# Performance work log

Hardware: AMD Instinct MI355X
Metric: run time of the kernel (lower is better)

Reference implementation:

```python
import jax, jax.numpy as jnp
import numpy as np

N, K, M, H, F = 4, 1024, 1024, 16, 4096
D = M // H  # per-head dim (dim_q = dim_v = 64)
EPS = 1e-5


def _mha(q_in, k_in, v_in, Wq, bq, Wk, bk, Wv, bv, Wo, bo, mask):
    # Wq/Wk/Wv: [H, M, D]; bq/bk/bv: [H, D]; Wo: [H*D, M]; bo: [M]
    q = jnp.einsum('nkm,hmd->nhkd', q_in, Wq) + bq[None, :, None, :]
    k = jnp.einsum('nkm,hmd->nhkd', k_in, Wk) + bk[None, :, None, :]
    v = jnp.einsum('nkm,hmd->nhkd', v_in, Wv) + bv[None, :, None, :]
    scores = jnp.einsum('nhkd,nhld->nhkl', q, k) / jnp.sqrt(jnp.asarray(D, q.dtype))
    if mask is not None:
        scores = jnp.where(mask[:, None, :, :] == 0, jnp.asarray(-jnp.inf, q.dtype), scores)
    attn = jax.nn.softmax(scores, axis=-1)          # [N,H,K,K]
    y = jnp.einsum('nhkl,nhld->nhkd', attn, v)      # [N,H,K,D]
    y = y.transpose(0, 2, 1, 3).reshape(q_in.shape[0], q_in.shape[1], -1)  # concat heads -> [N,K,H*D]
    return y @ Wo + bo


def _ln(x, g, b):
    mu = jnp.mean(x, axis=-1, keepdims=True)
    var = jnp.mean((x - mu) ** 2, axis=-1, keepdims=True)
    return (x - mu) * jax.lax.rsqrt(var + EPS) * g + b


def setup_inputs() -> dict:
    key = jax.random.key(0)
    ks = jax.random.split(key, 24)
    s = 0.02
    def rn(k, shape):
        return jax.random.normal(k, shape, dtype=jnp.float32) * s
    inp = {
        'dec_inp': jax.random.normal(ks[0], (N, K, M), dtype=jnp.float32),
        'enc_out': jax.random.normal(ks[1], (N, K, M), dtype=jnp.float32),
        'mask': jnp.tril(jnp.ones((K, K), dtype=jnp.int32))[None].repeat(N, axis=0),
        # self-attention params
        'Wq_s': rn(ks[2], (H, M, D)), 'bq_s': jnp.zeros((H, D)),
        'Wk_s': rn(ks[3], (H, M, D)), 'bk_s': jnp.zeros((H, D)),
        'Wv_s': rn(ks[4], (H, M, D)), 'bv_s': jnp.zeros((H, D)),
        'Wo_s': rn(ks[5], (H * D, M)), 'bo_s': jnp.zeros((M,)),
        # cross-attention params
        'Wq_c': rn(ks[6], (H, M, D)), 'bq_c': jnp.zeros((H, D)),
        'Wk_c': rn(ks[7], (H, M, D)), 'bk_c': jnp.zeros((H, D)),
        'Wv_c': rn(ks[8], (H, M, D)), 'bv_c': jnp.zeros((H, D)),
        'Wo_c': rn(ks[9], (H * D, M)), 'bo_c': jnp.zeros((M,)),
        # feedforward params
        'W1': rn(ks[10], (M, F)), 'b1': jnp.zeros((F,)),
        'W2': rn(ks[11], (F, M)), 'b2': jnp.zeros((M,)),
        # layernorm params
        'g1': jnp.ones((M,)), 'be1': jnp.zeros((M,)),
        'g2': jnp.ones((M,)), 'be2': jnp.zeros((M,)),
        'g3': jnp.ones((M,)), 'be3': jnp.zeros((M,)),
    }
    return inp


def reference(dec_inp, enc_out, mask,
              Wq_s, bq_s, Wk_s, bk_s, Wv_s, bv_s, Wo_s, bo_s,
              Wq_c, bq_c, Wk_c, bk_c, Wv_c, bv_c, Wo_c, bo_c,
              W1, b1, W2, b2, g1, be1, g2, be2, g3, be3):
    # masked self-attention + residual + LN (dropout = identity in eval)
    out1 = _mha(dec_inp, dec_inp, dec_inp, Wq_s, bq_s, Wk_s, bk_s, Wv_s, bv_s, Wo_s, bo_s, mask)
    out2 = _ln(dec_inp + out1, g1, be1)
    # cross-attention with encoder output + residual + LN
    out3 = _mha(out2, enc_out, enc_out, Wq_c, bq_c, Wk_c, bk_c, Wv_c, bv_c, Wo_c, bo_c, None)
    out4 = _ln(out3 + out2, g2, be2)
    # feedforward + residual + LN
    out5 = jax.nn.relu(out4 @ W1 + b1) @ W2 + b2
    return _ln(out5 + out4, g3, be3)
```

## Files before the change

### kernel.cpp

```cpp
#include <hip/hip_runtime.h>

#define NB   4
#define SEQ  1024
#define MD   1024
#define NH   16
#define HD   64
#define FF   4096
#define NK   (NB*SEQ)
#define EPSF 1e-5f
#define QS   3072

typedef short short8 __attribute__((ext_vector_type(8)));
typedef float f32x4  __attribute__((ext_vector_type(4)));
typedef unsigned short u16;
typedef unsigned int u32;

__device__ __forceinline__ u16 f2bf(float x) {
    union { float f; unsigned u; } v; v.f = x;
    unsigned r = v.u + 0x7FFF + ((v.u >> 16) & 1);
    return (u16)(r >> 16);
}
__device__ __forceinline__ u16 f2bf_trunc(float x) {
    union { float f; unsigned u; } v; v.f = x;
    return (u16)(v.u >> 16);
}
__device__ __forceinline__ float bf2f(u16 x) {
    union { unsigned u; float f; } v; v.u = ((unsigned)x) << 16;
    return v.f;
}
__device__ __forceinline__ void gload_lds16(const void* g, void* l) {
    __builtin_amdgcn_global_load_lds(
        (const __attribute__((address_space(1))) unsigned int*)g,
        (__attribute__((address_space(3))) unsigned int*)l,
        16, 0, 0);
}

__global__ __launch_bounds__(256) void conv_bf16(const float* __restrict__ s0,
                                                 const float* __restrict__ s1,
                                                 u16* __restrict__ d0,
                                                 u16* __restrict__ d1) {
    const float* S = blockIdx.y ? s1 : s0;
    u16* D = blockIdx.y ? d1 : d0;
    const int i = blockIdx.x * 256 + threadIdx.x;
    float4 v = ((const float4*)S)[i];
    ushort4 o;
    o.x = f2bf(v.x); o.y = f2bf(v.y); o.z = f2bf(v.z); o.w = f2bf(v.w);
    ((ushort4*)D)[i] = o;
}

__global__ __launch_bounds__(256) void mask_tiles(const int* __restrict__ mask,
                                                  int* __restrict__ cls,
                                                  u32* __restrict__ bits) {
    const int jt = blockIdx.x, qt = blockIdx.y, n = blockIdx.z;
    const int t = threadIdx.x;
    const int r = t >> 1, h2 = (t & 1) * 2;
    u32 bb[2];
#pragma unroll
    for (int sg = 0; sg < 2; ++sg) {
        const int* mp = &mask[((size_t)n * SEQ + qt * 128 + r) * SEQ + jt * 128 + (h2 + sg) * 32];
        u32 b = 0;
#pragma unroll
        for (int k = 0; k < 8; ++k) {
            int4 v = *(const int4*)(mp + k * 4);
            b |= (v.x ? 1u : 0u) << (k * 4 + 0);
            b |= (v.y ? 1u : 0u) << (k * 4 + 1);
            b |= (v.z ? 1u : 0u) << (k * 4 + 2);
            b |= (v.w ? 1u : 0u) << (k * 4 + 3);
        }
        bb[sg] = b;
    }
    const int tile = (n * 8 + qt) * 8 + jt;
    bits[((size_t)tile * 128 + r) * 4 + h2]     = bb[0];
    bits[((size_t)tile * 128 + r) * 4 + h2 + 1] = bb[1];
    const int nfull  = __syncthreads_count(bb[0] == 0xFFFFFFFFu && bb[1] == 0xFFFFFFFFu);
    const int nempty = __syncthreads_count(bb[0] == 0u && bb[1] == 0u);
    if (t == 0) cls[tile] = (nfull == 256) ? 2 : ((nempty == 256) ? 0 : 1);
}

struct QkvArgs { const float* src[6]; u16* dst[6]; };

__global__ __launch_bounds__(256) void repack_qkv(QkvArgs a) {
    const int m0 = blockIdx.x * 64;
    const int h  = blockIdx.y;
    const int w  = blockIdx.z;
    const float* W = a.src[w];
    u16* BT = a.dst[w];
    const int t = threadIdx.x;
    __shared__ u16 Ts[64][72];

    const int r = t >> 4, c4 = (t & 15) * 4;
#pragma unroll
    for (int p = 0; p < 4; ++p) {
        const int row = r + p * 16;
        float4 v = *(const float4*)&W[((size_t)h * 1024 + m0 + row) * 64 + c4];
        Ts[row][c4] = f2bf(v.x); Ts[row][c4 + 1] = f2bf(v.y);
        Ts[row][c4 + 2] = f2bf(v.z); Ts[row][c4 + 3] = f2bf(v.w);
    }
    __syncthreads();
    const int d = t >> 2, j0 = (t & 3) * 16;
#pragma unroll
    for (int p = 0; p < 4; ++p) {
        ushort4 o;
        o.x = Ts[j0 + p * 4 + 0][d]; o.y = Ts[j0 + p * 4 + 1][d];
        o.z = Ts[j0 + p * 4 + 2][d]; o.w = Ts[j0 + p * 4 + 3][d];
        *(ushort4*)&BT[((size_t)h * 64 + d) * 1024 + m0 + j0 + p * 4] = o;
    }
}

struct FD { const float* src; int ss; u16* dst; int ds; };
struct FlatArgs { FD d[10]; };

__global__ __launch_bounds__(256) void repack_flat(FlatArgs fa) {
    FD u = fa.d[blockIdx.z];
    const int r0 = blockIdx.x * 64;
    const int c0 = blockIdx.y * 64;
    const int t  = threadIdx.x;
    __shared__ u16 Ts[64][72];

    const int r = t >> 4, c4 = (t & 15) * 4;
#pragma unroll
    for (int p = 0; p < 4; ++p) {
        const int row = r + p * 16;
        float4 v = *(const float4*)&u.src[(size_t)(r0 + row) * u.ss + c0 + c4];
        Ts[row][c4] = f2bf(v.x); Ts[row][c4 + 1] = f2bf(v.y);
        Ts[row][c4 + 2] = f2bf(v.z); Ts[row][c4 + 3] = f2bf(v.w);
    }
    __syncthreads();
    const int d = t >> 2, j0 = (t & 3) * 16;
#pragma unroll
    for (int p = 0; p < 4; ++p) {
        ushort4 o;
        o.x = Ts[j0 + p * 4 + 0][d]; o.y = Ts[j0 + p * 4 + 1][d];
        o.z = Ts[j0 + p * 4 + 2][d]; o.w = Ts[j0 + p * 4 + 3][d];
        *(ushort4*)&u.dst[(size_t)(c0 + d) * u.ds + r0 + j0 + p * 4] = o;
    }
}

template<int OUT_BF16, int RELU, int RESID, int BIAS3, int PARTIAL, int VT>
__global__ __launch_bounds__(256) void gemm_mfma(const u16* __restrict__ A,
                                                 const u16* __restrict__ A2,
                                                 int Astride,
                                                 const u16* __restrict__ BT,
                                                 int Bstride,
                                                 const float* __restrict__ b0,
                                                 const float* __restrict__ b1p,
                                                 const float* __restrict__ b2p,
                                                 const float* __restrict__ resid,
                                                 void* __restrict__ Cout,
                                                 u16* __restrict__ VtOut,
                                                 int Kd, int Nd) {
    const int nt = blockIdx.x;
    const int mt = blockIdx.y;
    const int t  = threadIdx.x;
    const int wave = t >> 6, lane = t & 63;
    const int q = lane >> 4, l16 = lane & 15;
    const int wm = wave >> 1, wn = wave & 1;

    __shared__ __align__(16) u16 As[128 * 64];
    __shared__ __align__(16) u16 Bs[128 * 64];

    const int row0 = mt * 128, col0 = nt * 128;
    const u16* Ause = (col0 < 1024) ? A : A2;
    const int kBase = PARTIAL ? blockIdx.z * Kd : 0;

    f32x4 acc[4][4];
#pragma unroll
    for (int r = 0; r < 4; ++r)
#pragma unroll
        for (int c = 0; c < 4; ++c) acc[r][c] = (f32x4)0.0f;

    const int lrow = lane >> 3;
    const int lcb  = lane & 7;

    for (int k0 = 0; k0 < Kd; k0 += 64) {
        __syncthreads();
#pragma unroll
        for (int p = 0; p < 4; ++p) {
            const int rr = wave * 32 + p * 8 + lrow;
            const int gcb = lcb ^ (rr & 7);
            gload_lds16(Ause + (size_t)(row0 + rr) * Astride + kBase + k0 + gcb * 8, As + (size_t)(wave * 32 + p * 8) * 64);
            gload_lds16(BT   + (size_t)(col0 + rr) * Bstride + kBase + k0 + gcb * 8, Bs + (size_t)(wave * 32 + p * 8) * 64);
        }
        __syncthreads();

#pragma unroll
        for (int s = 0; s < 2; ++s) {
            const int pb = (q + s * 4) ^ (l16 & 7);
            short8 af[4], bf[4];
#pragma unroll
            for (int r = 0; r < 4; ++r)
                af[r] = *(const short8*)&As[(wm * 64 + r * 16 + l16) * 64 + pb * 8];
#pragma unroll
            for (int c = 0; c < 4; ++c)
                bf[c] = *(const short8*)&Bs[(wn * 64 + c * 16 + l16) * 64 + pb * 8];
#pragma unroll
            for (int r = 0; r < 4; ++r)
#pragma unroll
                for (int c = 0; c < 4; ++c)
                    acc[r][c] = __builtin_amdgcn_mfma_f32_16x16x32_bf16(af[r], bf[c], acc[r][c], 0, 0, 0);
        }
    }

    float* Pout = PARTIAL ? ((float*)Cout + (size_t)blockIdx.z * NK * Nd) : nullptr;

#pragma unroll
    for (int c = 0; c < 4; ++c) {
        const int col = col0 + wn * 64 + c * 16 + l16;
        float bb = 0.0f;
        if (!PARTIAL) {
            if (BIAS3) {
                const int sec = col >> 10;
                const float* bp = sec == 0 ? b0 : (sec == 1 ? b1p : b2p);
                bb = bp[col & 1023];
            } else {
                bb = b0[col];
            }
        }
#pragma unroll
        for (int r = 0; r < 4; ++r) {
#pragma unroll
            for (int reg = 0; reg < 4; ++reg) {
                const int row = row0 + wm * 64 + r * 16 + q * 4 + reg;
                float v = acc[r][c][reg] + bb;
                if (PARTIAL) {
                    Pout[(size_t)row * Nd + col] = acc[r][c][reg];
                } else {
                    if (RELU)  v = fmaxf(v, 0.0f);
                    if (RESID) v += resid[(size_t)row * Nd + col];
                    if (OUT_BF16) ((u16*)Cout)[(size_t)row * Nd + col] = f2bf(v);
                    else          ((float*)Cout)[(size_t)row * Nd + col] = v;
                }
            }
        }
    }
}

template<int OUT_BF16, int RELU, int BIAS3, int PARTIAL, int VT>
__global__ __launch_bounds__(512, 2) void gemm256(const u16* __restrict__ A,
                                                  const u16* __restrict__ A2,
                                                  int Astride,
                                                  const u16* __restrict__ BT,
                                                  int Bstride,
                                                  const float* __restrict__ b0,
                                                  const float* __restrict__ b1p,
                                                  const float* __restrict__ b2p,
                                                  void* __restrict__ Cout,
                                                  u16* __restrict__ VtOut,
                                                  int Kd, int Nd) {
    const int nt = blockIdx.x;
    const int mt = blockIdx.y;
    const int t  = threadIdx.x;
    const int wave = t >> 6, lane = t & 63;
    const int q = lane >> 4, l16 = lane & 15;
    const int wm = wave >> 2, wn = wave & 3;

    extern __shared__ __align__(16) char smem[];
    u16* As = (u16*)smem;
    u16* Bs = (u16*)(smem + 2 * 256 * 64 * 2);

    const int row0 = mt * 256, col0 = nt * 256;
    const u16* Ause = (col0 < 1024) ? A : A2;
    const int kBase = PARTIAL ? blockIdx.z * Kd : 0;

    f32x4 acc[8][4];
#pragma unroll
    for (int r = 0; r < 8; ++r)
#pragma unroll
        for (int c = 0; c < 4; ++c) acc[r][c] = (f32x4)0.0f;

    const int lrow = lane >> 3;
    const int lcb  = lane & 7;

    auto stage = [&](int buf, int kk) {
#pragma unroll
        for (int p = 0; p < 4; ++p) {
            const int rr = wave * 32 + p * 8 + lrow;
            const int gcb = lcb ^ (rr & 7);
            gload_lds16(Ause + (size_t)(row0 + rr) * Astride + kk + gcb * 8,
                        As + (size_t)buf * (256 * 64) + (wave * 32 + p * 8) * 64);
            gload_lds16(BT   + (size_t)(col0 + rr) * Bstride + kk + gcb * 8,
                        Bs + (size_t)buf * (256 * 64) + (wave * 32 + p * 8) * 64);
        }
    };

    const int nsteps = Kd / 64;
    stage(0, kBase);
    __syncthreads();

    int cur = 0;
    for (int it = 0; it < nsteps; ++it) {
        if (it + 1 < nsteps) stage(cur ^ 1, kBase + (it + 1) * 64);

        const u16* Ab = As + (size_t)cur * (256 * 64);
        const u16* Bb = Bs + (size_t)cur * (256 * 64);
#pragma unroll
        for (int s = 0; s < 2; ++s) {
            const int pb = (q + s * 4) ^ (l16 & 7);
            short8 af[8], bf[4];
#pragma unroll
            for (int r = 0; r < 8; ++r)
                af[r] = *(const short8*)&Ab[(wm * 128 + r * 16 + l16) * 64 + pb * 8];
#pragma unroll
            for (int c = 0; c < 4; ++c)
                bf[c] = *(const short8*)&Bb[(wn * 64 + c * 16 + l16) * 64 + pb * 8];
#pragma unroll
            for (int r = 0; r < 8; ++r)
#pragma unroll
                for (int c = 0; c < 4; ++c)
                    acc[r][c] = __builtin_amdgcn_mfma_f32_16x16x32_bf16(af[r], bf[c], acc[r][c], 0, 0, 0);
        }
        __syncthreads();
        cur ^= 1;
    }

    if (VT && col0 >= 2048) {
#pragma unroll
        for (int c = 0; c < 4; ++c) {
            const int col = col0 + wn * 64 + c * 16 + l16;
            const float bb = b2p[col & 1023];
            const int d = col & 63, hh = (col >> 6) & 15;
#pragma unroll
            for (int r = 0; r < 8; ++r) {
                const int row = row0 + wm * 128 + r * 16 + q * 4;
                const int nn = row >> 10, k = row & 1023;
                ushort4 o;
                o.x = f2bf(acc[r][c][0] + bb);
                o.y = f2bf(acc[r][c][1] + bb);
                o.z = f2bf(acc[r][c][2] + bb);
                o.w = f2bf(acc[r][c][3] + bb);
                *(ushort4*)&VtOut[((size_t)(nn * 16 + hh) * 64 + d) * 1024 + k] = o;
            }
        }
        return;
    }

    float* Pout = PARTIAL ? ((float*)Cout + (size_t)blockIdx.z * NK * Nd) : nullptr;

#pragma unroll
    for (int c = 0; c < 4; ++c) {
        const int col = col0 + wn * 64 + c * 16 + l16;
        float bb = 0.0f;
        if (!PARTIAL) {
            if (BIAS3) {
                const int sec = col >> 10;
                const float* bp = sec == 0 ? b0 : (sec == 1 ? b1p : b2p);
                bb = bp[col & 1023];
            } else {
                bb = b0[col];
            }
        }
#pragma unroll
        for (int r = 0; r < 8; ++r) {
#pragma unroll
            for (int reg = 0; reg < 4; ++reg) {
                const int row = row0 + wm * 128 + r * 16 + q * 4 + reg;
                float v = acc[r][c][reg] + bb;
                if (PARTIAL) {
                    Pout[(size_t)row * Nd + col] = acc[r][c][reg];
                } else {
                    if (RELU)  v = fmaxf(v, 0.0f);
                    if (OUT_BF16) ((u16*)Cout)[(size_t)row * Nd + col] = f2bf(v);
                    else          ((float*)Cout)[(size_t)row * Nd + col] = v;
                }
            }
        }
    }
}

#define PSTR 136
#define ATTN_LDS (128*64*2 + 64*128*2 + 8*16*PSTR*2)

__global__ __launch_bounds__(512, 4) void attn_mfma(const u16* __restrict__ QKV,
                                                    const u16* __restrict__ Vt,
                                                    const int* __restrict__ cls,
                                                    const u32* __restrict__ bits,
                                                    u16* __restrict__ Yout) {
    const int qt = blockIdx.x;
    const int h  = blockIdx.y;
    const int n  = blockIdx.z;
    const int t  = threadIdx.x;
    const int wave = t >> 6;
    const int lane = t & 63;
    const int quad = lane >> 4;
    const int l16  = lane & 15;
    const int sw   = wave >> 2;
    const int wq   = wave & 3;

    extern __shared__ __align__(16) char smem[];
    u16* Ks = (u16*)smem;
    u16* Vs = (u16*)(smem + 128 * 64 * 2);
    u16* Pw = (u16*)(smem + 128 * 64 * 2 + 64 * 128 * 2) + wave * 16 * PSTR;

    const int bh = n * NH + h;
    const int i0 = qt * 128;

    int cl[8];
    if (cls) {
        const int* cp = &cls[(n * 8 + qt) * 8];
#pragma unroll
        for (int j = 0; j < 8; ++j) cl[j] = cp[j];
    } else {
#pragma unroll
        for (int j = 0; j < 8; ++j) cl[j] = 2;
    }

    short8 qf[2];
    {
        const u16* qrow = QKV + ((size_t)n * SEQ + i0 + sw * 64 + wq * 16 + l16) * QS + h * 64 + quad * 8;
        short8 a = *(const short8*)(qrow);
        short8 b = *(const short8*)(qrow + 32);
#pragma unroll
        for (int j = 0; j < 8; ++j) {
            qf[0][j] = (short)f2bf(bf2f((u16)a[j]) * 0.18033688f);
            qf[1][j] = (short)f2bf(bf2f((u16)b[j]) * 0.18033688f);
        }
    }

    f32x4 O[4];
#pragma unroll
    for (int d = 0; d < 4; ++d) O[d] = (f32x4)0.0f;
    float lrow[4] = {};

    const int krow = lane >> 3, kblk = lane & 7;
    const int vrow = lane >> 4, vblk = lane & 15;
    const int x7 = l16 & 7;

    for (int jt = 0; jt < SEQ / 128; ++jt) {
        const int c = cl[jt];
        if (c == 0) continue;
        __syncthreads();

#pragma unroll
        for (int p = 0; p < 2; ++p) {
            const int rr = wave * 16 + p * 8 + krow;
            const int kb = kblk ^ (rr & 7);
            gload_lds16(QKV + ((size_t)n * SEQ + jt * 128 + rr) * QS + 1024 + h * 64 + kb * 8,
                        Ks + (wave * 16 + p * 8) * 64);
        }
#pragma unroll
        for (int p = 0; p < 2; ++p) {
            const int rr = wave * 8 + p * 4 + vrow;
            const int kb = vblk ^ (rr & 15);
            gload_lds16(Vt + ((size_t)bh * HD + rr) * SEQ + jt * 128 + kb * 8,
                        Vs + (wave * 8 + p * 4) * 128);
        }
        __syncthreads();

        f32x4 S[8];
#pragma unroll
        for (int sub = 0; sub < 8; ++sub) {
            S[sub] = (f32x4)0.0f;
            const int row = sub * 16 + l16;
            short8 k0 = *(const short8*)&Ks[row * 64 + ((quad ^ x7) * 8)];
            S[sub] = __builtin_amdgcn_mfma_f32_16x16x32_bf16(qf[0], k0, S[sub], 0, 0, 0);
            short8 k1 = *(const short8*)&Ks[row * 64 + (((4 + quad) ^ x7) * 8)];
            S[sub] = __builtin_amdgcn_mfma_f32_16x16x32_bf16(qf[1], k1, S[sub], 0, 0, 0);
        }

        if (c == 1) {
#pragma unroll
            for (int reg = 0; reg < 4; ++reg) {
                const int row = sw * 64 + wq * 16 + quad * 4 + reg;
                const uint4 mm = *(const uint4*)&bits[((size_t)((n * 8 + qt) * 8 + jt) * 128 + row) * 4];
#pragma unroll
                for (int sub = 0; sub < 8; ++sub) {
                    const u32 seg = (sub >> 1) == 0 ? mm.x : (sub >> 1) == 1 ? mm.y : (sub >> 1) == 2 ? mm.z : mm.w;
                    if (!((seg >> ((sub & 1) * 16 + l16)) & 1u)) S[sub][reg] = -1e30f;
                }
            }
        }

#pragma unroll
        for (int reg = 0; reg < 4; ++reg) {
            float rs = 0.0f;
#pragma unroll
            for (int sub = 0; sub < 8; ++sub) {
                float e = exp2f(S[sub][reg]);
                Pw[(quad * 4 + reg) * PSTR + sub * 16 + l16] = f2bf_trunc(e);
                rs += e;
            }
            rs += __shfl_xor(rs, 1);
            rs += __shfl_xor(rs, 2);
            rs += __shfl_xor(rs, 4);
            rs += __shfl_xor(rs, 8);
            lrow[reg] += rs;
        }

        short8 pa[4];
#pragma unroll
        for (int ks = 0; ks < 4; ++ks)
            pa[ks] = *(const short8*)&Pw[l16 * PSTR + ks * 32 + quad * 8];
#pragma unroll
        for (int d = 0; d < 4; ++d) {
            const int row = d * 16 + l16;
#pragma unroll
            for (int ks = 0; ks < 4; ++ks) {
                short8 vb = *(const short8*)&Vs[row * 128 + (((ks * 4 + quad) ^ l16) & 15) * 8];
                O[d] = __builtin_amdgcn_mfma_f32_16x16x32_bf16(pa[ks], vb, O[d], 0, 0, 0);
            }
        }
    }

#pragma unroll
    for (int d = 0; d < 4; ++d) {
#pragma unroll
        for (int reg = 0; reg < 4; ++reg) {
            const int row = i0 + sw * 64 + wq * 16 + quad * 4 + reg;
            const int col = h * 64 + d * 16 + l16;
            Yout[((size_t)n * SEQ + row) * QS + col] = f2bf(O[d][reg] / lrow[reg]);
        }
    }
}

__global__ __launch_bounds__(256) void ln_kernel(const float* __restrict__ X,
                                                 const float* __restrict__ g,
                                                 const float* __restrict__ be,
                                                 float* __restrict__ Y,
                                                 u16* __restrict__ Yb) {
    const int row = blockIdx.x;
    const int t = threadIdx.x;
    __shared__ float red[256];

    const float4 v = ((const float4*)(X + (size_t)row * MD))[t];
    red[t] = v.x + v.y + v.z + v.w;
    __syncthreads();
    for (int s2 = 128; s2 > 0; s2 >>= 1) {
        if (t < s2) red[t] += red[t + s2];
        __syncthreads();
    }
    const float mu = red[0] * (1.0f / MD);
    __syncthreads();

    float dx = v.x - mu, dy = v.y - mu, dz = v.z - mu, dw = v.w - mu;
    red[t] = dx * dx + dy * dy + dz * dz + dw * dw;
    __syncthreads();
    for (int s2 = 128; s2 > 0; s2 >>= 1) {
        if (t < s2) red[t] += red[t + s2];
        __syncthreads();
    }
    const float var = red[0] * (1.0f / MD);
    const float rs = rsqrtf(var + EPSF);

    const float4 gv = ((const float4*)g)[t];
    const float4 bv = ((const float4*)be)[t];
    float4 o;
    o.x = dx * rs * gv.x + bv.x;
    o.y = dy * rs * gv.y + bv.y;
    o.z = dz * rs * gv.z + bv.z;
    o.w = dw * rs * gv.w + bv.w;
    if (Y) ((float4*)(Y + (size_t)row * MD))[t] = o;
    if (Yb) {
        ushort4 ob;
        ob.x = f2bf(o.x); ob.y = f2bf(o.y); ob.z = f2bf(o.z); ob.w = f2bf(o.w);
        ((ushort4*)(Yb + (size_t)row * MD))[t] = ob;
    }
}

__global__ __launch_bounds__(256) void ln_fused2(const float* __restrict__ p0,
                                                 const float* __restrict__ p1,
                                                 const float* __restrict__ bias,
                                                 const float* __restrict__ resid,
                                                 const float* __restrict__ g,
                                                 const float* __restrict__ be,
                                                 float* __restrict__ Y) {
    const int row = blockIdx.x;
    const int t = threadIdx.x;
    __shared__ float red[256];

    const float4 a = ((const float4*)(p0 + (size_t)row * MD))[t];
    const float4 b = ((const float4*)(p1 + (size_t)row * MD))[t];
    const float4 r = ((const float4*)(resid + (size_t)row * MD))[t];
    const float4 bi = ((const float4*)bias)[t];
    float4 v;
    v.x = a.x + b.x + r.x + bi.x;
    v.y = a.y + b.y + r.y + bi.y;
    v.z = a.z + b.z + r.z + bi.z;
    v.w = a.w + b.w + r.w + bi.w;

    red[t] = v.x + v.y + v.z + v.w;
    __syncthreads();
    for (int s2 = 128; s2 > 0; s2 >>= 1) {
        if (t < s2) red[t] += red[t + s2];
        __syncthreads();
    }
    const float mu = red[0] * (1.0f / MD);
    __syncthreads();

    float dx = v.x - mu, dy = v.y - mu, dz = v.z - mu, dw = v.w - mu;
    red[t] = dx * dx + dy * dy + dz * dz + dw * dw;
    __syncthreads();
    for (int s2 = 128; s2 > 0; s2 >>= 1) {
        if (t < s2) red[t] += red[t + s2];
        __syncthreads();
    }
    const float var = red[0] * (1.0f / MD);
    const float rs = rsqrtf(var + EPSF);

    const float4 gv = ((const float4*)g)[t];
    const float4 bv = ((const float4*)be)[t];
    float4 o;
    o.x = dx * rs * gv.x + bv.x;
    o.y = dy * rs * gv.y + bv.y;
    o.z = dz * rs * gv.z + bv.z;
    o.w = dw * rs * gv.w + bv.w;
    ((float4*)(Y + (size_t)row * MD))[t] = o;
}

extern "C" void kernel_launch(void* const* d_in, const int* in_sizes, int n_in,
                              void* d_out, int out_size, void* d_ws, size_t ws_size,
                              hipStream_t stream) {
    const float* dec  = (const float*)d_in[0];
    const float* enc  = (const float*)d_in[1];
    const int*   mask = (const int*)d_in[2];
    const float* Wq_s = (const float*)d_in[3];
    const float* bq_s = (const float*)d_in[4];
    const float* Wk_s = (const float*)d_in[5];
    const float* bk_s = (const float*)d_in[6];
    const float* Wv_s = (const float*)d_in[7];
    const float* bv_s = (const float*)d_in[8];
    const float* Wo_s = (const float*)d_in[9];
    const float* bo_s = (const float*)d_in[10];
    const float* Wq_c = (const float*)d_in[11];
    const float* bq_c = (const float*)d_in[12];
    const float* Wk_c = (const float*)d_in[13];
    const float* bk_c = (const float*)d_in[14];
    const float* Wv_c = (const float*)d_in[15];
    const float* bv_c = (const float*)d_in[16];
    const float* Wo_c = (const float*)d_in[17];
    const float* bo_c = (const float*)d_in[18];
    const float* W1   = (const float*)d_in[19];
    const float* b1   = (const float*)d_in[20];
    const float* W2   = (const float*)d_in[21];
    const float* b2   = (const float*)d_in[22];
    const float* g1   = (const float*)d_in[23];
    const float* be1  = (const float*)d_in[24];
    const float* g2   = (const float*)d_in[25];
    const float* be2  = (const float*)d_in[26];
    const float* g3   = (const float*)d_in[27];
    const float* be3  = (const float*)d_in[28];

    char* wsb = (char*)d_ws;
    const size_t MB = 1u << 20;
    u16*   decb  = (u16*)(wsb + 0 * MB);
    u16*   O2b   = (u16*)(wsb + 0 * MB);
    u16*   encb  = (u16*)(wsb + 8 * MB);
    u16*   O4b   = (u16*)(wsb + 8 * MB);
    u16*   WqkvsT= (u16*)(wsb + 16 * MB);
    u16*   WqkvcT= (u16*)(wsb + 22 * MB);
    u16*   WosT  = (u16*)(wsb + 28 * MB);
    u16*   WocT  = (u16*)(wsb + 30 * MB);
    u16*   W1T   = (u16*)(wsb + 32 * MB);
    u16*   W2T   = (u16*)(wsb + 40 * MB);
    u16*   QKVb  = (u16*)(wsb + 48 * MB);
    u16*   Vt    = (u16*)(wsb + 72 * MB);
    u16*   Hb    = (u16*)(wsb + 48 * MB);
    int*   mcls  = (int*)(wsb + 80 * MB);
    u32*   mbits = (u32*)(wsb + 80 * MB + 64 * 1024);
    float* Tb    = (float*)(wsb + 80 * MB);
    float* FP    = (float*)(wsb + 0 * MB);
    float* O2    = (float*)(wsb + 96 * MB);
    float* O4    = (float*)(wsb + 96 * MB);

    dim3 blk(256);
    dim3 blkA(512);
    dim3 blkG(512);
    dim3 gConv(NK * MD / 4 / 256, 2);
    dim3 gMask(8, 8, 4);
    dim3 gQkvW(16, 16, 6);
    dim3 gFlatW(16, 16, 10);
    dim3 gAttn(SEQ / 128, NH, NB);
    dim3 gQKV(QS / 256, NK / 256);
    dim3 gOut(MD / 128, NK / 128);
    dim3 gF1(FF / 256, NK / 256);
    dim3 gF2(MD / 256, NK / 256, 2);
    const int G256_LDS = 2 * 2 * 256 * 64 * 2;

    conv_bf16<<<gConv, blk, 0, stream>>>(dec, enc, decb, encb);
    mask_tiles<<<gMask, blk, 0, stream>>>(mask, mcls, mbits);

    QkvArgs qa;
    qa.src[0] = Wq_s; qa.src[1] = Wk_s; qa.src[2] = Wv_s;
    qa.src[3] = Wq_c; qa.src[4] = Wk_c; qa.src[5] = Wv_c;
    qa.dst[0] = WqkvsT;                 qa.dst[1] = WqkvsT + (size_t)1024 * 1024;
    qa.dst[2] = WqkvsT + (size_t)2048 * 1024;
    qa.dst[3] = WqkvcT;                 qa.dst[4] = WqkvcT + (size_t)1024 * 1024;
    qa.dst[5] = WqkvcT + (size_t)2048 * 1024;
    repack_qkv<<<gQkvW, blk, 0, stream>>>(qa);

    FlatArgs fa;
    fa.d[0] = { Wo_s, 1024, WosT, 1024 };
    fa.d[1] = { Wo_c, 1024, WocT, 1024 };
    for (int u = 0; u < 4; ++u)
        fa.d[2 + u] = { W1 + (size_t)u * 1024, 4096, W1T + (size_t)u * 1024 * 1024, 1024 };
    for (int u = 0; u < 4; ++u)
        fa.d[6 + u] = { W2 + (size_t)u * 1024 * 1024, 1024, W2T + (size_t)u * 1024, 4096 };
    repack_flat<<<gFlatW, blk, 0, stream>>>(fa);

    gemm256<1, 0, 1, 0, 1><<<gQKV, blkG, G256_LDS, stream>>>(decb, decb, MD, WqkvsT, MD, bq_s, bk_s, bv_s, QKVb, Vt, MD, QS);
    attn_mfma<<<gAttn, blkA, ATTN_LDS, stream>>>(QKVb, Vt, mcls, mbits, QKVb);
    gemm_mfma<0, 0, 1, 0, 0, 0><<<gOut, blk, 0, stream>>>(QKVb, QKVb, QS, WosT, MD, bo_s, nullptr, nullptr, dec, Tb, nullptr, MD, MD);
    ln_kernel<<<NK, blk, 0, stream>>>(Tb, g1, be1, O2, O2b);

    gemm256<1, 0, 1, 0, 1><<<gQKV, blkG, G256_LDS, stream>>>(O2b, encb, MD, WqkvcT, MD, bq_c, bk_c, bv_c, QKVb, Vt, MD, QS);
    attn_mfma<<<gAttn, blkA, ATTN_LDS, stream>>>(QKVb, Vt, nullptr, nullptr, QKVb);
    gemm_mfma<0, 0, 1, 0, 0, 0><<<gOut, blk, 0, stream>>>(QKVb, QKVb, QS, WocT, MD, bo_c, nullptr, nullptr, O2, Tb, nullptr, MD, MD);
    ln_kernel<<<NK, blk, 0, stream>>>(Tb, g2, be2, O4, O4b);

    gemm256<1, 1, 0, 0, 0><<<gF1, blkG, G256_LDS, stream>>>(O4b, O4b, MD, W1T, MD, b1, nullptr, nullptr, Hb, nullptr, MD, FF);
    gemm256<0, 0, 0, 1, 0><<<gF2, blkG, G256_LDS, stream>>>(Hb, Hb, FF, W2T, FF, nullptr, nullptr, nullptr, FP, nullptr, FF / 2, MD);
    ln_fused2<<<NK, blk, 0, stream>>>(FP, FP + (size_t)NK * MD, b2, O4, g3, be3, (float*)d_out);
}
```

Before: 356.0 us.

## Add XCD-aware block swizzle, fine-grained vmcnt waits, and BN=128 tile for FF2

The GEMM kernel remaps block indices so that neighbouring tiles land on the same XCD, aiming for better L2 reuse. The full __syncthreads is replaced with explicit s_waitcnt vmcnt counts plus raw barriers, so the next stage's global-to-LDS loads stay in flight while compute runs. The kernel also gains a BN template parameter, and the second FFN GEMM uses 128-wide N tiles to double its block count. The swizzle assumes the grid divides evenly by 8 and by swzW, and the hand-counted waits depend on the exact number of loads issued per stage.

```diff
diff --git a/kernel.cpp b/kernel.cpp
--- a/kernel.cpp
+++ b/kernel.cpp
@@ -235,7 +235,7 @@
     }
 }
 
-template<int OUT_BF16, int RELU, int BIAS3, int PARTIAL, int VT>
+template<int BN, int OUT_BF16, int RELU, int BIAS3, int PARTIAL, int VT>
 __global__ __launch_bounds__(512, 2) void gemm256(const u16* __restrict__ A,
                                                   const u16* __restrict__ A2,
                                                   int Astride,
@@ -246,27 +246,36 @@
                                                   const float* __restrict__ b2p,
                                                   void* __restrict__ Cout,
                                                   u16* __restrict__ VtOut,
-                                                  int Kd, int Nd) {
-    const int nt = blockIdx.x;
-    const int mt = blockIdx.y;
+                                                  int Kd, int Nd, int swzW) {
     const int t  = threadIdx.x;
     const int wave = t >> 6, lane = t & 63;
     const int q = lane >> 4, l16 = lane & 15;
     const int wm = wave >> 2, wn = wave & 3;
+    constexpr int NC = BN / 64;
+
+    const int gx = gridDim.x;
+    const int bid = blockIdx.x + blockIdx.y * gx;
+    const int cpx = (gx * gridDim.y) >> 3;
+    const int xcd = bid & 7;
+    const int cc  = bid >> 3;
+    const int regNX = gx / swzW;
+    const int mtspan = cpx / swzW;
+    const int nt = (xcd % regNX) * swzW + cc % swzW;
+    const int mt = (xcd / regNX) * mtspan + cc / swzW;
 
     extern __shared__ __align__(16) char smem[];
     u16* As = (u16*)smem;
     u16* Bs = (u16*)(smem + 2 * 256 * 64 * 2);
 
-    const int row0 = mt * 256, col0 = nt * 256;
+    const int row0 = mt * 256, col0 = nt * BN;
     const u16* Ause = (col0 < 1024) ? A : A2;
     const int kBase = PARTIAL ? blockIdx.z * Kd : 0;
 
-    f32x4 acc[8][4];
+    f32x4 acc[8][NC];
 #pragma unroll
     for (int r = 0; r < 8; ++r)
 #pragma unroll
-        for (int c = 0; c < 4; ++c) acc[r][c] = (f32x4)0.0f;
+        for (int c = 0; c < NC; ++c) acc[r][c] = (f32x4)0.0f;
 
     const int lrow = lane >> 3;
     const int lcb  = lane & 7;
@@ -278,45 +287,57 @@
             const int gcb = lcb ^ (rr & 7);
             gload_lds16(Ause + (size_t)(row0 + rr) * Astride + kk + gcb * 8,
                         As + (size_t)buf * (256 * 64) + (wave * 32 + p * 8) * 64);
-            gload_lds16(BT   + (size_t)(col0 + rr) * Bstride + kk + gcb * 8,
-                        Bs + (size_t)buf * (256 * 64) + (wave * 32 + p * 8) * 64);
+        }
+#pragma unroll
+        for (int p = 0; p < BN / 64; ++p) {
+            const int rr = wave * (BN / 8) + p * 8 + lrow;
+            const int gcb = lcb ^ (rr & 7);
+            gload_lds16(BT + (size_t)(col0 + rr) * Bstride + kk + gcb * 8,
+                        Bs + (size_t)buf * (BN * 64) + (wave * (BN / 8) + p * 8) * 64);
         }
     };
 
     const int nsteps = Kd / 64;
     stage(0, kBase);
-    __syncthreads();
 
     int cur = 0;
     for (int it = 0; it < nsteps; ++it) {
-        if (it + 1 < nsteps) stage(cur ^ 1, kBase + (it + 1) * 64);
+        const bool pre = (it + 1 < nsteps);
+        if (pre) {
+            stage(cur ^ 1, kBase + (it + 1) * 64);
+            if constexpr (BN == 256) asm volatile("s_waitcnt vmcnt(8)" ::: "memory");
+            else                     asm volatile("s_waitcnt vmcnt(6)" ::: "memory");
+        } else {
+            asm volatile("s_waitcnt vmcnt(0)" ::: "memory");
+        }
+        __builtin_amdgcn_s_barrier();
 
         const u16* Ab = As + (size_t)cur * (256 * 64);
-        const u16* Bb = Bs + (size_t)cur * (256 * 64);
+        const u16* Bb = Bs + (size_t)cur * (BN * 64);
 #pragma unroll
         for (int s = 0; s < 2; ++s) {
             const int pb = (q + s * 4) ^ (l16 & 7);
-            short8 af[8], bf[4];
+            short8 af[8], bf[NC];
 #pragma unroll
             for (int r = 0; r < 8; ++r)
                 af[r] = *(const short8*)&Ab[(wm * 128 + r * 16 + l16) * 64 + pb * 8];
 #pragma unroll
-            for (int c = 0; c < 4; ++c)
-                bf[c] = *(const short8*)&Bb[(wn * 64 + c * 16 + l16) * 64 + pb * 8];
+            for (int c = 0; c < NC; ++c)
+                bf[c] = *(const short8*)&Bb[(wn * (BN / 4) + c * 16 + l16) * 64 + pb * 8];
 #pragma unroll
             for (int r = 0; r < 8; ++r)
 #pragma unroll
-                for (int c = 0; c < 4; ++c)
+                for (int c = 0; c < NC; ++c)
                     acc[r][c] = __builtin_amdgcn_mfma_f32_16x16x32_bf16(af[r], bf[c], acc[r][c], 0, 0, 0);
         }
-        __syncthreads();
+        __builtin_amdgcn_s_barrier();
         cur ^= 1;
     }
 
     if (VT && col0 >= 2048) {
 #pragma unroll
-        for (int c = 0; c < 4; ++c) {
-            const int col = col0 + wn * 64 + c * 16 + l16;
+        for (int c = 0; c < NC; ++c) {
+            const int col = col0 + wn * (BN / 4) + c * 16 + l16;
             const float bb = b2p[col & 1023];
             const int d = col & 63, hh = (col >> 6) & 15;
 #pragma unroll
@@ -337,8 +358,8 @@
     float* Pout = PARTIAL ? ((float*)Cout + (size_t)blockIdx.z * NK * Nd) : nullptr;
 
 #pragma unroll
-    for (int c = 0; c < 4; ++c) {
-        const int col = col0 + wn * 64 + c * 16 + l16;
+    for (int c = 0; c < NC; ++c) {
+        const int col = col0 + wn * (BN / 4) + c * 16 + l16;
         float bb = 0.0f;
         if (!PARTIAL) {
             if (BIAS3) {
@@ -672,8 +693,9 @@
     dim3 gQKV(QS / 256, NK / 256);
     dim3 gOut(MD / 128, NK / 128);
     dim3 gF1(FF / 256, NK / 256);
-    dim3 gF2(MD / 256, NK / 256, 2);
-    const int G256_LDS = 2 * 2 * 256 * 64 * 2;
+    dim3 gF2(MD / 128, NK / 256, 2);
+    const int G256_LDS  = 2 * (256 + 256) * 64 * 2;
+    const int G128_LDS  = 2 * (256 + 128) * 64 * 2;
 
     conv_bf16<<<gConv, blk, 0, stream>>>(dec, enc, decb, encb);
     mask_tiles<<<gMask, blk, 0, stream>>>(mask, mcls, mbits);
@@ -696,17 +718,17 @@
         fa.d[6 + u] = { W2 + (size_t)u * 1024 * 1024, 1024, W2T + (size_t)u * 1024, 4096 };
     repack_flat<<<gFlatW, blk, 0, stream>>>(fa);
 
-    gemm256<1, 0, 1, 0, 1><<<gQKV, blkG, G256_LDS, stream>>>(decb, decb, MD, WqkvsT, MD, bq_s, bk_s, bv_s, QKVb, Vt, MD, QS);
+    gemm256<256, 1, 0, 1, 0, 1><<<gQKV, blkG, G256_LDS, stream>>>(decb, decb, MD, WqkvsT, MD, bq_s, bk_s, bv_s, QKVb, Vt, MD, QS, 3);
     attn_mfma<<<gAttn, blkA, ATTN_LDS, stream>>>(QKVb, Vt, mcls, mbits, QKVb);
     gemm_mfma<0, 0, 1, 0, 0, 0><<<gOut, blk, 0, stream>>>(QKVb, QKVb, QS, WosT, MD, bo_s, nullptr, nullptr, dec, Tb, nullptr, MD, MD);
     ln_kernel<<<NK, blk, 0, stream>>>(Tb, g1, be1, O2, O2b);
 
-    gemm256<1, 0, 1, 0, 1><<<gQKV, blkG, G256_LDS, stream>>>(O2b, encb, MD, WqkvcT, MD, bq_c, bk_c, bv_c, QKVb, Vt, MD, QS);
+    gemm256<256, 1, 0, 1, 0, 1><<<gQKV, blkG, G256_LDS, stream>>>(O2b, encb, MD, WqkvcT, MD, bq_c, bk_c, bv_c, QKVb, Vt, MD, QS, 3);
     attn_mfma<<<gAttn, blkA, ATTN_LDS, stream>>>(QKVb, Vt, nullptr, nullptr, QKVb);
     gemm_mfma<0, 0, 1, 0, 0, 0><<<gOut, blk, 0, stream>>>(QKVb, QKVb, QS, WocT, MD, bo_c, nullptr, nullptr, O2, Tb, nullptr, MD, MD);
     ln_kernel<<<NK, blk, 0, stream>>>(Tb, g2, be2, O4, O4b);
 
-    gemm256<1, 1, 0, 0, 0><<<gF1, blkG, G256_LDS, stream>>>(O4b, O4b, MD, W1T, MD, b1, nullptr, nullptr, Hb, nullptr, MD, FF);
-    gemm256<0, 0, 0, 1, 0><<<gF2, blkG, G256_LDS, stream>>>(Hb, Hb, FF, W2T, FF, nullptr, nullptr, nullptr, FP, nullptr, FF / 2, MD);
+    gemm256<256, 1, 1, 0, 0, 0><<<gF1, blkG, G256_LDS, stream>>>(O4b, O4b, MD, W1T, MD, b1, nullptr, nullptr, Hb, nullptr, MD, FF, 4);
+    gemm256<128, 0, 0, 0, 1, 0><<<gF2, blkG, G128_LDS, stream>>>(Hb, Hb, FF, W2T, FF, nullptr, nullptr, nullptr, FP, nullptr, FF / 2, MD, 2);
     ln_fused2<<<NK, blk, 0, stream>>>(FP, FP + (size_t)NK * MD, b2, O4, g3, be3, (float*)d_out);
 }
```

Measured after the change: 351.4 us. No clear change (-1.3%).
